# Performance work log

Measured on AMD Instinct MI355X. Metric: run time of the kernel, lower is better.

Reference implementation:

```python
import jax, jax.numpy as jnp
import numpy as np

C = 256          # channels
KS = 7           # kernel_size
G = 256          # groups (defaults to channels)
HID = C // 4     # hidden = channels // reduction
BN_EPS = 1e-5


def setup_inputs() -> dict:
    key = jax.random.key(0)
    ks = jax.random.split(key, 4)
    B, H, W = 4, 64, 64
    return {
        "x": jax.random.normal(ks[0], (B, C, H, W), jnp.float32),
        "reduce_w": jax.random.normal(ks[1], (HID, C), jnp.float32) / np.float32(np.sqrt(C)),
        "bn_gamma": jnp.ones((HID,), jnp.float32),
        "bn_beta": jnp.zeros((HID,), jnp.float32),
        "bn_mean": jnp.zeros((HID,), jnp.float32),
        "bn_var": jnp.ones((HID,), jnp.float32),
        "kproj_w": jax.random.normal(ks[2], (KS * KS * G, HID), jnp.float32) / np.float32(np.sqrt(HID)),
        "kproj_b": jnp.zeros((KS * KS * G,), jnp.float32),
    }


def _kernels(x, reduce_w, bn_gamma, bn_beta, bn_mean, bn_var, kproj_w, kproj_b):
    # 1x1 conv -> BN (eval mode) -> ReLU -> 1x1 conv, then per-pixel L2 kernel norm
    B, _, H, W = x.shape
    h = jnp.einsum('bchw,oc->bohw', x, reduce_w)
    inv = bn_gamma / jnp.sqrt(bn_var + BN_EPS)
    h = h * inv[None, :, None, None] + (bn_beta - bn_mean * inv)[None, :, None, None]
    h = jax.nn.relu(h)
    ker = jnp.einsum('bchw,oc->bohw', h, kproj_w) + kproj_b[None, :, None, None]
    ker = ker.reshape(B, G, KS * KS, H, W)           # (B, G, k*k, H, W)
    # kernel_norm == 'l2': zero-mean + unit L2 norm over the k*k taps
    ker = ker - ker.mean(axis=2, keepdims=True)
    denom = jnp.maximum(jnp.sqrt(jnp.sum(ker * ker, axis=2, keepdims=True)), 1e-6)
    return ker / denom


def reference(x, reduce_w, bn_gamma, bn_beta, bn_mean, bn_var, kproj_w, kproj_b):
    # get_kernels is under @torch.no_grad() in the original -> stop_gradient
    ker = jax.lax.stop_gradient(
        _kernels(x, reduce_w, bn_gamma, bn_beta, bn_mean, bn_var, kproj_w, kproj_b))
    B, Cc, H, W = x.shape
    pad = KS // 2
    gc = Cc // G  # = 1 for depthwise involution
    xp = jnp.pad(x, ((0, 0), (0, 0), (pad, pad), (pad, pad)))
    xg = xp.reshape(B, G, gc, H + 2 * pad, W + 2 * pad)
    # fused unfold-multiply-accumulate over the k*k taps (no (B,C,k,k,H,W) tensor)
    out = jnp.zeros((B, G, gc, H, W), x.dtype)
    for t in range(KS * KS):
        i, j = divmod(t, KS)
        out = out + xg[:, :, :, i:i + H, j:j + W] * ker[:, :, t][:, :, None]
    return out.reshape(B, Cc, H, W)
```

## Files before the change

kernel.cpp:

```cpp
#include <hip/hip_runtime.h>


#define C_    256
#define HID_  64
#define KS_   7
#define KK_   49
#define G_    256
#define H_    64
#define W_    64
#define HW_   4096
#define BN_EPS 1e-5f

typedef __attribute__((ext_vector_type(8))) short bf16x8;
typedef __attribute__((ext_vector_type(4))) float f32x4;

__device__ __forceinline__ ushort f2bf(float f) {
    unsigned u = __float_as_uint(f);
    return (ushort)((u + 0x7fffu + ((u >> 16) & 1u)) >> 16);
}
__device__ __forceinline__ float bf2f(ushort s) {
    return __uint_as_float((unsigned)s << 16);
}

__global__ __launch_bounds__(256) void prep_kernel(
    const float* __restrict__ kw, const float* __restrict__ kb,
    const float* __restrict__ reduce_w,
    const float* __restrict__ bn_gamma, const float* __restrict__ bn_beta,
    const float* __restrict__ bn_mean, const float* __restrict__ bn_var,
    ushort* __restrict__ kwb, float* __restrict__ rwT, float* __restrict__ betp,
    float* __restrict__ kbp)
{
    const int bid = blockIdx.x;
    if (bid < 256) {
        int idx  = bid * 256 + threadIdx.x;
        int base = idx * 16;
        int g    = base >> 12;
        int rem  = base & 4095;
        int t    = rem >> 6;
        int k0   = rem & 63;
        if (t == 49 || t == 50) return;
        union { ushort s[16]; uint4 v[2]; } u;
        if (t < KK_) {
            const float* src = kw + ((size_t)(g * KK_ + t)) * HID_ + k0;
            #pragma unroll
            for (int i = 0; i < 16; ++i) u.s[i] = f2bf(src[i]);
        } else {
            #pragma unroll
            for (int i = 0; i < 16; ++i) u.s[i] = 0;
        }
        uint4* dst = (uint4*)(kwb + base);
        dst[0] = u.v[0];
        dst[1] = u.v[1];
    } else if (bid == 256) {
        int k = threadIdx.x;
        #pragma unroll 1
        for (int o = 0; o < HID_; ++o) {
            float inv = bn_gamma[o] * rsqrtf(bn_var[o] + BN_EPS);
            rwT[k * HID_ + o] = reduce_w[o * C_ + k] * inv;
        }
        if (k < HID_) {
            float inv = bn_gamma[k] * rsqrtf(bn_var[k] + BN_EPS);
            betp[k] = bn_beta[k] - bn_mean[k] * inv;
        }
    } else if (bid == 257) {
        for (int i = threadIdx.x; i < G_ * 64; i += 256) {
            int g = i >> 6, t = i & 63;
            if (t == 49) continue;
            kbp[i] = (t < KK_) ? kb[g * KK_ + t] : 0.f;
        }
    } else {
        const int g = bid - 258;
        __shared__ float part[4][64];
        const int k  = threadIdx.x & 63;
        const int pr = threadIdx.x >> 6;
        const int t0 = pr * 13;
        const int t1 = (t0 + 13 < KK_) ? t0 + 13 : KK_;
        float s = 0.f;
        for (int t = t0; t < t1; ++t)
            s += kw[((size_t)(g * KK_ + t)) * HID_ + k];
        part[pr][k] = s;
        __syncthreads();
        if (threadIdx.x < 64) {
            float u = part[0][k] + part[1][k] + part[2][k] + part[3][k];
            ushort uh = f2bf(u);
            ushort ul = f2bf(u - bf2f(uh));
            kwb[(size_t)g * 4096 + 49 * 64 + k] = uh;
            kwb[(size_t)g * 4096 + 50 * 64 + k] = ul;
            float bs = (k < KK_) ? kb[g * KK_ + k] : 0.f;
            #pragma unroll
            for (int off = 32; off >= 1; off >>= 1) bs += __shfl_xor(bs, off);
            if (k == 0) kbp[g * 64 + 49] = bs;
        }
    }
}

__global__ __launch_bounds__(256) void hv1_kernel(
    const float* __restrict__ x, const float* __restrict__ rwT,
    float* __restrict__ hvp, int npx)
{
    const int lane = threadIdx.x & 63;
    const int wq   = __builtin_amdgcn_readfirstlane(threadIdx.x >> 6);
    const int kq   = blockIdx.y;
    const int p    = blockIdx.x * 64 + lane;
    const int b    = p >> 12;
    const int hw   = p & 4095;

    float acc[16];
    #pragma unroll
    for (int j = 0; j < 16; ++j) acc[j] = 0.f;

    const float* xp = x + ((size_t)b * C_ + kq * 64) * HW_ + hw;
    const float* rw = rwT + (kq * 64) * HID_ + wq * 16;
    #pragma unroll 8
    for (int kk = 0; kk < 64; ++kk) {
        float xk = xp[(size_t)kk * HW_];
        #pragma unroll
        for (int j = 0; j < 16; ++j) acc[j] = fmaf(xk, rw[kk * HID_ + j], acc[j]);
    }
    float* dst = hvp + ((size_t)(kq * 64 + wq * 16)) * npx + p;
    #pragma unroll
    for (int j = 0; j < 16; ++j) dst[(size_t)j * npx] = acc[j];
}

__global__ __launch_bounds__(256) void hv2_kernel(
    const float* __restrict__ hvp, const float* __restrict__ betp,
    ushort* __restrict__ hv, int npx)
{
    const int p  = blockIdx.x * 256 + threadIdx.x;
    const int o0 = blockIdx.y * 4;
    ushort s[4];
    #pragma unroll
    for (int j = 0; j < 4; ++j) {
        float v = 0.f;
        #pragma unroll
        for (int kq = 0; kq < 4; ++kq)
            v += hvp[(size_t)(kq * 64 + o0 + j) * npx + p];
        s[j] = f2bf(fmaxf(v + betp[o0 + j], 0.f));
    }
    uint2 w;
    w.x = (uint)s[0] | ((uint)s[1] << 16);
    w.y = (uint)s[2] | ((uint)s[3] << 16);
    *(uint2*)(hv + (size_t)p * HID_ + o0) = w;
}

__global__ __launch_bounds__(256) void invol_main(
    const float* __restrict__ x, const ushort* __restrict__ hv,
    const ushort* __restrict__ kwb, const float* __restrict__ kbp,
    float* __restrict__ out)
{
    __shared__ float x_s[38][72];

    const int tid  = threadIdx.x;
    const int lane = tid & 63;
    const int wave = __builtin_amdgcn_readfirstlane(tid >> 6);
    const int bg   = blockIdx.x;
    const int b    = bg >> 8;
    const int g    = bg & 255;
    const int y0   = blockIdx.y << 5;
    const int l15  = lane & 15;
    const int l4   = lane >> 4;

    const float* xg = x + (size_t)bg * HW_;
    for (int idx = tid; idx < 38 * 72; idx += 256) {
        int r = idx / 72, c = idx - r * 72;
        int yy = y0 - 3 + r;
        int yc = yy < 0 ? 0 : (yy > 63 ? 63 : yy);
        int cc = c - 3;
        x_s[r][c] = ((unsigned)cc < 64u) ? xg[yc * 64 + cc] : 0.f;
    }

    bf16x8 ka[2][4];
    const char* kwg = (const char*)kwb + (size_t)g * 8192;
    #pragma unroll
    for (int ks = 0; ks < 2; ++ks)
        #pragma unroll
        for (int tm = 0; tm < 4; ++tm) {
            int byte = (tm * 16 + l15) * 128 + ks * 64 + l4 * 16;
            ka[ks][tm] = *(const bf16x8*)(kwg + byte);
        }
    f32x4 kv[4];
    #pragma unroll
    for (int tm = 0; tm < 4; ++tm)
        kv[tm] = *(const f32x4*)(kbp + g * 64 + tm * 16 + l4 * 4);

    int po[3][4];
    int im3[3][4];
    #pragma unroll
    for (int tm = 0; tm < 3; ++tm)
        #pragma unroll
        for (int r = 0; r < 4; ++r) {
            int t = tm * 16 + l4 * 4 + r;
            int i = (t * 147) >> 10;
            int j = t - i * 7;
            po[tm][r]  = i * 72 + l15 + j;
            im3[tm][r] = i - 3;
        }
    const int po48 = 6 * 72 + l15 + 6;

    __syncthreads();

    const int rowpix0 = (b << 12) + (y0 << 6);

    #pragma unroll 2
    for (int rr = 0; rr < 8; ++rr) {
        const int ry = rr * 4 + wave;
        const int y  = y0 + ry;

        bf16x8 hb[2][4];
        #pragma unroll
        for (int ks = 0; ks < 2; ++ks)
            #pragma unroll
            for (int pn = 0; pn < 4; ++pn) {
                const char* p = (const char*)(hv +
                    (size_t)(rowpix0 + (ry << 6) + pn * 16 + l15) * HID_)
                    + ks * 64 + l4 * 16;
                hb[ks][pn] = *(const bf16x8*)p;
            }

        f32x4 acc[4][4];
        #pragma unroll
        for (int tm = 0; tm < 4; ++tm)
            #pragma unroll
            for (int pn = 0; pn < 4; ++pn) acc[tm][pn] = (f32x4)(0.f);
        #pragma unroll
        for (int ks = 0; ks < 2; ++ks)
            #pragma unroll
            for (int tm = 0; tm < 4; ++tm)
                #pragma unroll
                for (int pn = 0; pn < 4; ++pn)
                    acc[tm][pn] = __builtin_amdgcn_mfma_f32_16x16x32_bf16(
                        ka[ks][tm], hb[ks][pn], acc[tm][pn], 0, 0, 0);

        #pragma unroll
        for (int tm = 0; tm < 4; ++tm)
            #pragma unroll
            for (int pn = 0; pn < 4; ++pn)
                #pragma unroll
                for (int r = 0; r < 4; ++r) acc[tm][pn][r] += kv[tm][r];

        float m_all[4], inv_[4];
        #pragma unroll
        for (int pn = 0; pn < 4; ++pn) {
            float ssq = 0.f;
            #pragma unroll
            for (int tm = 0; tm < 3; ++tm)
                #pragma unroll
                for (int r = 0; r < 4; ++r) {
                    float e = acc[tm][pn][r];
                    ssq = fmaf(e, e, ssq);
                }
            float e48 = acc[3][pn][0];
            ssq += (l4 == 0) ? e48 * e48 : 0.f;
            ssq += __shfl_xor(ssq, 16);
            ssq += __shfl_xor(ssq, 32);
            float mr = acc[3][pn][1] + acc[3][pn][2];
            float m  = __shfl(mr, l15) * (1.f / 49.f);
            float ss = fmaxf(ssq - 49.f * m * m, 0.f);
            m_all[pn] = m;
            inv_[pn]  = 1.f / fmaxf(sqrtf(ss), 1e-6f);
        }

        float kx[4] = {0.f, 0.f, 0.f, 0.f};
        float xs[4] = {0.f, 0.f, 0.f, 0.f};
        const float* xrow = &x_s[ry][0];
        #pragma unroll
        for (int tm = 0; tm < 3; ++tm)
            #pragma unroll
            for (int r = 0; r < 4; ++r) {
                const bool  rok  = (unsigned)(y + im3[tm][r]) < 64u;
                const float* bp  = xrow + po[tm][r];
                #pragma unroll
                for (int pn = 0; pn < 4; ++pn) {
                    float xv = bp[pn * 16];
                    xv = rok ? xv : 0.f;
                    kx[pn] = fmaf(acc[tm][pn][r], xv, kx[pn]);
                    xs[pn] += xv;
                }
            }
        {
            const bool  rok48 = ((y + 3) < 64) && (l4 == 0);
            const float* bp   = xrow + po48;
            #pragma unroll
            for (int pn = 0; pn < 4; ++pn) {
                float xv = bp[pn * 16];
                xv = rok48 ? xv : 0.f;
                kx[pn] = fmaf(acc[3][pn][0], xv, kx[pn]);
                xs[pn] += xv;
            }
        }
        float ov[4];
        #pragma unroll
        for (int pn = 0; pn < 4; ++pn) {
            float k2 = kx[pn];
            k2 += __shfl_xor(k2, 16);
            k2 += __shfl_xor(k2, 32);
            float x2 = xs[pn];
            x2 += __shfl_xor(x2, 16);
            x2 += __shfl_xor(x2, 32);
            ov[pn] = (k2 - m_all[pn] * x2) * inv_[pn];
        }
        float outv = (l4 == 0) ? ov[0] : (l4 == 1) ? ov[1] : (l4 == 2) ? ov[2] : ov[3];
        out[(size_t)bg * HW_ + (y << 6) + lane] = outv;
    }
}

__global__ __launch_bounds__(256) void hv_kernel(
    const float* __restrict__ x, const float* __restrict__ rwT,
    const float* __restrict__ betp, ushort* __restrict__ hv)
{
    const int lane = threadIdx.x & 63;
    const int q    = __builtin_amdgcn_readfirstlane(threadIdx.x >> 6);
    const int p    = blockIdx.x * 64 + lane;
    const int b    = p >> 12;
    const int hw   = p & 4095;
    float acc[16];
    #pragma unroll
    for (int j = 0; j < 16; ++j) acc[j] = betp[q * 16 + j];
    const float* xp = x + (size_t)b * C_ * HW_ + hw;
    #pragma unroll 8
    for (int k = 0; k < C_; ++k) {
        float xk = xp[(size_t)k * HW_];
        const float* rw = rwT + k * HID_ + q * 16;
        #pragma unroll
        for (int j = 0; j < 16; ++j) acc[j] = fmaf(xk, rw[j], acc[j]);
    }
    union { ushort s[16]; uint4 v[2]; } u;
    #pragma unroll
    for (int j = 0; j < 16; ++j) u.s[j] = f2bf(fmaxf(acc[j], 0.f));
    uint4* dst = (uint4*)(hv + (size_t)p * HID_ + q * 16);
    dst[0] = u.v[0];
    dst[1] = u.v[1];
}

__global__ __launch_bounds__(256) void invol_fallback(
    const float* __restrict__ x, const float* __restrict__ reduce_w,
    const float* __restrict__ bn_gamma, const float* __restrict__ bn_beta,
    const float* __restrict__ bn_mean, const float* __restrict__ bn_var,
    const float* __restrict__ kw, const float* __restrict__ kb,
    float* __restrict__ out)
{
    __shared__ float rwT[C_][HID_ + 4];
    __shared__ float bns[HID_];
    __shared__ float bnb[HID_];
    const int tid = threadIdx.x;
    const int b  = blockIdx.z;
    const int g0 = blockIdx.y * 32;
    const int p  = blockIdx.x * 256 + tid;
    const int py = p >> 6;
    const int px = p & 63;
    #pragma unroll 1
    for (int o = 0; o < HID_; ++o) rwT[tid][o] = reduce_w[o * C_ + tid];
    if (tid < HID_) {
        float inv = bn_gamma[tid] * rsqrtf(bn_var[tid] + BN_EPS);
        bns[tid] = inv;
        bnb[tid] = bn_beta[tid] - bn_mean[tid] * inv;
    }
    __syncthreads();
    float hvv[HID_];
    #pragma unroll
    for (int o = 0; o < HID_; ++o) hvv[o] = 0.f;
    const float* xb = x + (size_t)b * C_ * HW_ + p;
    #pragma unroll 4
    for (int k = 0; k < C_; ++k) {
        float xk = xb[(size_t)k * HW_];
        const float4* wr = (const float4*)&rwT[k][0];
        #pragma unroll
        for (int o4 = 0; o4 < HID_ / 4; ++o4) {
            float4 w = wr[o4];
            hvv[o4*4+0] = fmaf(xk, w.x, hvv[o4*4+0]);
            hvv[o4*4+1] = fmaf(xk, w.y, hvv[o4*4+1]);
            hvv[o4*4+2] = fmaf(xk, w.z, hvv[o4*4+2]);
            hvv[o4*4+3] = fmaf(xk, w.w, hvv[o4*4+3]);
        }
    }
    #pragma unroll
    for (int o = 0; o < HID_; ++o) hvv[o] = fmaxf(fmaf(hvv[o], bns[o], bnb[o]), 0.f);
    #pragma unroll 1
    for (int gi = 0; gi < 32; ++gi) {
        const int g = g0 + gi;
        const float* kwg = kw + (size_t)g * KK_ * HID_;
        float acc[KK_];
        #pragma unroll
        for (int t = 0; t < KK_; ++t) {
            float a = kb[g * KK_ + t];
            const float4* row = (const float4*)(kwg + t * HID_);
            #pragma unroll
            for (int k4 = 0; k4 < HID_ / 4; ++k4) {
                float4 w = row[k4];
                a = fmaf(w.x, hvv[k4*4+0], a);
                a = fmaf(w.y, hvv[k4*4+1], a);
                a = fmaf(w.z, hvv[k4*4+2], a);
                a = fmaf(w.w, hvv[k4*4+3], a);
            }
            acc[t] = a;
        }
        float mean = 0.f;
        #pragma unroll
        for (int t = 0; t < KK_; ++t) mean += acc[t];
        mean *= (1.f / 49.f);
        float ss = 0.f;
        #pragma unroll
        for (int t = 0; t < KK_; ++t) { acc[t] -= mean; ss = fmaf(acc[t], acc[t], ss); }
        float inv = 1.f / fmaxf(sqrtf(ss), 1e-6f);
        const float* xg = x + ((size_t)(b * G_ + g)) * HW_;
        float oacc = 0.f;
        #pragma unroll
        for (int i = 0; i < KS_; ++i) {
            int yv = py + i - 3;
            bool rok = ((unsigned)yv < (unsigned)H_);
            const float* xrow = xg + yv * W_;
            #pragma unroll
            for (int j = 0; j < KS_; ++j) {
                int xx = px + j - 3;
                bool ok = rok && ((unsigned)xx < (unsigned)W_);
                float v = ok ? xrow[xx] : 0.f;
                oacc = fmaf(v, acc[i*7+j], oacc);
            }
        }
        out[((size_t)(b * G_ + g)) * HW_ + p] = oacc * inv;
    }
}

extern "C" void kernel_launch(void* const* d_in, const int* in_sizes, int n_in,
                              void* d_out, int out_size, void* d_ws, size_t ws_size,
                              hipStream_t stream) {
    const float* x        = (const float*)d_in[0];
    const float* reduce_w = (const float*)d_in[1];
    const float* bn_gamma = (const float*)d_in[2];
    const float* bn_beta  = (const float*)d_in[3];
    const float* bn_mean  = (const float*)d_in[4];
    const float* bn_var   = (const float*)d_in[5];
    const float* kproj_w  = (const float*)d_in[6];
    const float* kproj_b  = (const float*)d_in[7];
    float* out = (float*)d_out;
    const int B   = in_sizes[0] / (C_ * HW_);
    const int npx = B * HW_;

    size_t kwb_off = 0;
    size_t kwb_sz  = (size_t)G_ * 64 * 64 * 2;
    size_t kbp_off = kwb_off + kwb_sz;
    size_t kbp_sz  = (size_t)G_ * 64 * 4;
    size_t rwt_off = kbp_off + kbp_sz;
    size_t rwt_sz  = (size_t)C_ * HID_ * 4;
    size_t bet_off = rwt_off + rwt_sz;
    size_t bet_sz  = 256;
    size_t hv_off  = bet_off + bet_sz;
    size_t hv_sz   = (size_t)npx * HID_ * 2;
    size_t hvp_off = hv_off + hv_sz;
    size_t hvp_sz  = (size_t)4 * HID_ * npx * 4;
    size_t need2   = hvp_off;
    size_t need    = hvp_off + hvp_sz;

    if (ws_size < need2) {
        dim3 grid(HW_ / 256, G_ / 32, B);
        invol_fallback<<<grid, 256, 0, stream>>>(x, reduce_w, bn_gamma, bn_beta,
                                                 bn_mean, bn_var, kproj_w, kproj_b, out);
        return;
    }

    ushort* kwb  = (ushort*)((char*)d_ws + kwb_off);
    float*  kbp  = (float*)((char*)d_ws + kbp_off);
    float*  rwT  = (float*)((char*)d_ws + rwt_off);
    float*  betp = (float*)((char*)d_ws + bet_off);
    ushort* hv   = (ushort*)((char*)d_ws + hv_off);
    float*  hvp  = (float*)((char*)d_ws + hvp_off);

    prep_kernel<<<dim3(258 + G_), 256, 0, stream>>>(kproj_w, kproj_b, reduce_w,
                                                    bn_gamma, bn_beta, bn_mean, bn_var,
                                                    kwb, rwT, betp, kbp);
    if (ws_size >= need) {
        hv1_kernel<<<dim3(npx / 64, 4), 256, 0, stream>>>(x, rwT, hvp, npx);
        hv2_kernel<<<dim3(npx / 256, 16), 256, 0, stream>>>(hvp, betp, hv, npx);
    } else {
        hv_kernel<<<dim3(npx / 64), 256, 0, stream>>>(x, rwT, betp, hv);
    }
    invol_main<<<dim3(B * G_, 2), 256, 0, stream>>>(x, hv, kwb, kbp, out);
}
```

Before: 151.3 us.

## Precompute 7x7 window sums of x in shared memory and fold bias into MFMA

```diff
diff --git a/kernel.cpp b/kernel.cpp
--- a/kernel.cpp
+++ b/kernel.cpp
@@ -149,6 +149,8 @@
     float* __restrict__ out)
 {
     __shared__ float x_s[38][72];
+    __shared__ float hs_s[38][64];
+    __shared__ float vs_s[32][64];
 
     const int tid  = threadIdx.x;
     const int lane = tid & 63;
@@ -164,9 +166,9 @@
     for (int idx = tid; idx < 38 * 72; idx += 256) {
         int r = idx / 72, c = idx - r * 72;
         int yy = y0 - 3 + r;
-        int yc = yy < 0 ? 0 : (yy > 63 ? 63 : yy);
         int cc = c - 3;
-        x_s[r][c] = ((unsigned)cc < 64u) ? xg[yc * 64 + cc] : 0.f;
+        bool v = ((unsigned)yy < 64u) && ((unsigned)cc < 64u);
+        x_s[r][c] = v ? xg[yy * 64 + cc] : 0.f;
     }
 
     bf16x8 ka[2][4];
@@ -184,7 +186,6 @@
         kv[tm] = *(const f32x4*)(kbp + g * 64 + tm * 16 + l4 * 4);
 
     int po[3][4];
-    int im3[3][4];
     #pragma unroll
     for (int tm = 0; tm < 3; ++tm)
         #pragma unroll
@@ -192,11 +193,39 @@
             int t = tm * 16 + l4 * 4 + r;
             int i = (t * 147) >> 10;
             int j = t - i * 7;
-            po[tm][r]  = i * 72 + l15 + j;
-            im3[tm][r] = i - 3;
+            po[tm][r] = i * 72 + l15 + j;
         }
     const int po48 = 6 * 72 + l15 + 6;
 
+    __syncthreads();
+
+    if (tid < 152) {
+        int r  = tid >> 2;
+        int c0 = (tid & 3) << 4;
+        float s = 0.f;
+        #pragma unroll
+        for (int j = 0; j < 7; ++j) s += x_s[r][c0 + j];
+        hs_s[r][c0] = s;
+        #pragma unroll
+        for (int c = 1; c < 16; ++c) {
+            s += x_s[r][c0 + c + 6] - x_s[r][c0 + c - 1];
+            hs_s[r][c0 + c] = s;
+        }
+    }
+    __syncthreads();
+    {
+        int c   = tid & 63;
+        int ry0 = (tid >> 6) << 3;
+        float s = 0.f;
+        #pragma unroll
+        for (int i = 0; i < 7; ++i) s += hs_s[ry0 + i][c];
+        vs_s[ry0][c] = s;
+        #pragma unroll
+        for (int k = 1; k < 8; ++k) {
+            s += hs_s[ry0 + k + 6][c] - hs_s[ry0 + k - 1][c];
+            vs_s[ry0 + k][c] = s;
+        }
+    }
     __syncthreads();
 
     const int rowpix0 = (b << 12) + (y0 << 6);
@@ -221,7 +250,7 @@
         #pragma unroll
         for (int tm = 0; tm < 4; ++tm)
             #pragma unroll
-            for (int pn = 0; pn < 4; ++pn) acc[tm][pn] = (f32x4)(0.f);
+            for (int pn = 0; pn < 4; ++pn) acc[tm][pn] = kv[tm];
         #pragma unroll
         for (int ks = 0; ks < 2; ++ks)
             #pragma unroll
@@ -230,13 +259,6 @@
                 for (int pn = 0; pn < 4; ++pn)
                     acc[tm][pn] = __builtin_amdgcn_mfma_f32_16x16x32_bf16(
                         ka[ks][tm], hb[ks][pn], acc[tm][pn], 0, 0, 0);
-
-        #pragma unroll
-        for (int tm = 0; tm < 4; ++tm)
-            #pragma unroll
-            for (int pn = 0; pn < 4; ++pn)
-                #pragma unroll
-                for (int r = 0; r < 4; ++r) acc[tm][pn][r] += kv[tm][r];
 
         float m_all[4], inv_[4];
         #pragma unroll
@@ -250,7 +272,7 @@
                     ssq = fmaf(e, e, ssq);
                 }
             float e48 = acc[3][pn][0];
-            ssq += (l4 == 0) ? e48 * e48 : 0.f;
+            ssq = fmaf(e48, e48, ssq);
             ssq += __shfl_xor(ssq, 16);
             ssq += __shfl_xor(ssq, 32);
             float mr = acc[3][pn][1] + acc[3][pn][2];
@@ -261,46 +283,35 @@
         }
 
         float kx[4] = {0.f, 0.f, 0.f, 0.f};
-        float xs[4] = {0.f, 0.f, 0.f, 0.f};
         const float* xrow = &x_s[ry][0];
         #pragma unroll
         for (int tm = 0; tm < 3; ++tm)
             #pragma unroll
             for (int r = 0; r < 4; ++r) {
-                const bool  rok  = (unsigned)(y + im3[tm][r]) < 64u;
-                const float* bp  = xrow + po[tm][r];
+                const float* bp = xrow + po[tm][r];
                 #pragma unroll
-                for (int pn = 0; pn < 4; ++pn) {
-                    float xv = bp[pn * 16];
-                    xv = rok ? xv : 0.f;
-                    kx[pn] = fmaf(acc[tm][pn][r], xv, kx[pn]);
-                    xs[pn] += xv;
-                }
+                for (int pn = 0; pn < 4; ++pn)
+                    kx[pn] = fmaf(acc[tm][pn][r], bp[pn * 16], kx[pn]);
             }
         {
-            const bool  rok48 = ((y + 3) < 64) && (l4 == 0);
-            const float* bp   = xrow + po48;
-            #pragma unroll
-            for (int pn = 0; pn < 4; ++pn) {
-                float xv = bp[pn * 16];
-                xv = rok48 ? xv : 0.f;
-                kx[pn] = fmaf(acc[3][pn][0], xv, kx[pn]);
-                xs[pn] += xv;
-            }
-        }
-        float ov[4];
+            const float* bp = xrow + po48;
+            #pragma unroll
+            for (int pn = 0; pn < 4; ++pn)
+                kx[pn] = fmaf(acc[3][pn][0], bp[pn * 16], kx[pn]);
+        }
+        float k2[4];
         #pragma unroll
         for (int pn = 0; pn < 4; ++pn) {
-            float k2 = kx[pn];
-            k2 += __shfl_xor(k2, 16);
-            k2 += __shfl_xor(k2, 32);
-            float x2 = xs[pn];
-            x2 += __shfl_xor(x2, 16);
-            x2 += __shfl_xor(x2, 32);
-            ov[pn] = (k2 - m_all[pn] * x2) * inv_[pn];
-        }
-        float outv = (l4 == 0) ? ov[0] : (l4 == 1) ? ov[1] : (l4 == 2) ? ov[2] : ov[3];
-        out[(size_t)bg * HW_ + (y << 6) + lane] = outv;
+            float v = kx[pn];
+            v += __shfl_xor(v, 16);
+            v += __shfl_xor(v, 32);
+            k2[pn] = v;
+        }
+        float k2s = (l4 == 0) ? k2[0] : (l4 == 1) ? k2[1] : (l4 == 2) ? k2[2] : k2[3];
+        float ms  = (l4 == 0) ? m_all[0] : (l4 == 1) ? m_all[1] : (l4 == 2) ? m_all[2] : m_all[3];
+        float is  = (l4 == 0) ? inv_[0] : (l4 == 1) ? inv_[1] : (l4 == 2) ? inv_[2] : inv_[3];
+        float x2  = vs_s[ry][lane];
+        out[(size_t)bg * HW_ + (y << 6) + lane] = (k2s - ms * x2) * is;
     }
 }
 
```

Measured after the change: 148.8 us. No clear change (-1.7%).
